# Performance work log

Hardware: AMD Instinct MI355X
Metric: run time of the kernel (lower is better)

The kernel has to match this reference:

```python
import jax, jax.numpy as jnp
import numpy as np

N_HEADS = 16
PROJ_DIM = 64  # per-head dim
DIM = N_HEADS * PROJ_DIM  # 1024


def setup_inputs() -> dict:
    key = jax.random.key(0)
    k1, k2, k3, k4, k5 = jax.random.split(key, 5)
    N, L = 2, 2048
    scale = 1.0 / np.sqrt(DIM)
    return {
        "query": jax.random.normal(k1, (N, L, DIM), dtype=jnp.float32),
        "key": jax.random.normal(k2, (N, L, DIM), dtype=jnp.float32),
        "Wq": jax.random.normal(k3, (DIM, DIM), dtype=jnp.float32) * scale,
        "Wk": jax.random.normal(k4, (DIM, DIM), dtype=jnp.float32) * scale,
        "Wv": jax.random.normal(k5, (DIM, DIM), dtype=jnp.float32) * scale,
    }


def reference(query, key, Wq, Wk, Wv):
    # Causal linear-complexity attention (mask=True branch, left_first=False).
    N, Lq, _ = query.shape
    Lk = key.shape[1]
    H, Dh = N_HEADS, PROJ_DIM
    # torch Linear: x @ W.T ; reshape to (N, H, L, Dh)
    q = (query @ Wq.T).reshape(N, Lq, H, Dh).transpose(0, 2, 1, 3)
    k = (key @ Wk.T).reshape(N, Lk, H, Dh).transpose(0, 2, 1, 3)
    v = (key @ Wv.T).reshape(N, Lk, H, Dh).transpose(0, 2, 1, 3)
    q = jax.nn.softmax(q, axis=-1)
    k = jax.nn.softmax(k, axis=-1)
    # right[t] = sum_{s<=t} k_s^T v_s  : (N,H,Lk,Dh,Dh) cumulative outer products
    S = jnp.cumsum(jnp.einsum('nhti,nhtj->nhtij', k, v), axis=2)
    out = jnp.einsum('nhti,nhtij->nhtj', q, S)  # (N,H,Lq,Dh)
    return out.transpose(0, 2, 1, 3).reshape(N, Lq, H * Dh)
```

## Files before the change

### kernel.cpp

```cpp
#include <hip/hip_runtime.h>


constexpr int DIM  = 1024;
constexpr int H    = 16;
constexpr int DH   = 64;
constexpr int LSEQ = 2048;
constexpr int NB   = 2;
constexpr int MTOK = NB * LSEQ;
constexpr int CS   = 64;
constexpr int NC   = LSEQ / CS;
constexpr int SEG  = 8;
constexpr int CPS  = NC / SEG;

typedef __bf16 bf16x8 __attribute__((ext_vector_type(8)));
typedef float floatx4 __attribute__((ext_vector_type(4)));
typedef unsigned short ushort_t;

__device__ __forceinline__ ushort_t f2bf(float f) {
  unsigned int u = __float_as_uint(f);
  u += 0x7FFFu + ((u >> 16) & 1u);
  return (ushort_t)(u >> 16);
}

__device__ __forceinline__ void async16(void* lds, const void* g) {
  __builtin_amdgcn_global_load_lds(
      (const __attribute__((address_space(1))) unsigned int*)g,
      (__attribute__((address_space(3))) unsigned int*)lds, 16, 0, 0);
}

__device__ __forceinline__ bf16x8 tfrag(const unsigned int* T, int row, int uoff) {
  union { bf16x8 v; unsigned int u[4]; } r;
  const unsigned int* p = T + row * 33 + uoff;
  r.u[0] = p[0]; r.u[1] = p[1]; r.u[2] = p[2]; r.u[3] = p[3];
  return r.v;
}

__device__ __forceinline__ void transpose_tile(const ushort_t* g, unsigned int* TT, int tid) {
  const int ic = tid & 7, tp = tid >> 3;
  const ushort_t* r0 = g + (size_t)(2 * tp) * DIM + ic * 8;
  union { uint4 q; ushort_t u[8]; } a0, a1;
  a0.q = *(const uint4*)r0;
  a1.q = *(const uint4*)(r0 + DIM);
#pragma unroll
  for (int j = 0; j < 8; j++)
    TT[(8 * ic + j) * 33 + tp] = (unsigned int)a0.u[j] | ((unsigned int)a1.u[j] << 16);
}

__global__ __launch_bounds__(256) void cast_all(const float* __restrict__ q,
                                                const float* __restrict__ k,
                                                const float* __restrict__ wq,
                                                const float* __restrict__ wk,
                                                const float* __restrict__ wv,
                                                ushort_t* __restrict__ xbf,
                                                ushort_t* __restrict__ wbf) {
  const int seg = blockIdx.y;
  const float* src;
  ushort_t* dst;
  int n4;
  if (seg == 0)      { src = q;  dst = xbf;                  n4 = (4 << 20) / 4; }
  else if (seg == 1) { src = k;  dst = xbf + (4 << 20);      n4 = (4 << 20) / 4; }
  else if (seg == 2) { src = wq; dst = wbf;                  n4 = (1 << 20) / 4; }
  else if (seg == 3) { src = wk; dst = wbf + (1 << 20);      n4 = (1 << 20) / 4; }
  else               { src = wv; dst = wbf + (2 << 20);      n4 = (1 << 20) / 4; }
  for (int i = blockIdx.x * 256 + threadIdx.x; i < n4; i += gridDim.x * 256) {
    const float4 f = ((const float4*)src)[i];
    ((ushort4*)dst)[i] = make_ushort4(f2bf(f.x), f2bf(f.y), f2bf(f.z), f2bf(f.w));
  }
}

__global__ __launch_bounds__(512, 2) void gemm_fused(const ushort_t* __restrict__ xbf,
                                                     const ushort_t* __restrict__ wbf,
                                                     ushort_t* __restrict__ qp,
                                                     ushort_t* __restrict__ kp,
                                                     ushort_t* __restrict__ vp) {
  __shared__ __align__(16) ushort_t sh[65536];
  const int tid = threadIdx.x;

  const int xcd   = blockIdx.x & 7;
  const int local = blockIdx.x >> 3;
  const int T     = xcd * 24 + local;
  const int z     = T >> 6;
  const int rem   = T & 63;
  const int bm    = (rem >> 2) * 256;
  const int bn    = (rem & 3) * 256;

  const ushort_t* A = xbf + (z ? (size_t)(4 << 20) : 0);
  const ushort_t* W = wbf + (size_t)z * (1 << 20);
  ushort_t* C = (z == 0) ? qp : ((z == 1) ? kp : vp);

  const int lane  = tid & 63;
  const int wid   = tid >> 6;
  const int wr    = wid >> 2, wc = wid & 3;
  const int row16 = lane & 15, quad = lane >> 4;

  floatx4 acc[8][4] = {};

  const int srow = tid >> 3;
  const int lc   = (tid & 7) ^ (srow & 7);
  const ushort_t* pA[2][2];
  const ushort_t* pB[2][2];
#pragma unroll
  for (int h = 0; h < 2; h++)
#pragma unroll
    for (int rnd = 0; rnd < 2; rnd++) {
      pA[h][rnd] = A + (size_t)(bm + h * 128 + rnd * 64 + srow) * DIM + lc * 8;
      pB[h][rnd] = W + (size_t)(bn + h * 128 + rnd * 64 + srow) * DIM + lc * 8;
    }
  char* shW = (char*)sh;

#define STG(b, ism, h, kt)                                          \
  {                                                                 \
    char* d_ = shW + (b) * 65536 + (ism) * 32768 + (h) * 16384 + tid * 16; \
    async16(d_,        ((ism) ? pB : pA)[h][0] + (size_t)(kt) * 64);       \
    async16(d_ + 8192, ((ism) ? pB : pA)[h][1] + (size_t)(kt) * 64);       \
  }

  const int key = row16 & 7;
  const int xc0 = (quad ^ key) * 16;
  const int xc1 = ((4 + quad) ^ key) * 16;
  const int aOff = wr * 16384 + row16 * 128;
  const int bOff = 32768 + (wc >> 1) * 16384 + (wc & 1) * 8192 + row16 * 128;
  const char* shR = (const char*)sh;

  bf16x8 aF[4][2], bF[4][2];

#define RD_A4(p, base)                                                        \
  {                                                                           \
    _Pragma("unroll")                                                         \
    for (int mt = 0; mt < 4; mt++) {                                          \
      aF[mt][0] = *(const bf16x8*)(shR + (p) * 65536 + aOff + ((base) + mt) * 2048 + xc0); \
      aF[mt][1] = *(const bf16x8*)(shR + (p) * 65536 + aOff + ((base) + mt) * 2048 + xc1); \
    }                                                                         \
  }
#define RD_B2(p, base)                                                        \
  {                                                                           \
    _Pragma("unroll")                                                         \
    for (int j = 0; j < 2; j++) {                                             \
      bF[(base) + j][0] = *(const bf16x8*)(shR + (p) * 65536 + bOff + ((base) + j) * 2048 + xc0); \
      bF[(base) + j][1] = *(const bf16x8*)(shR + (p) * 65536 + bOff + ((base) + j) * 2048 + xc1); \
    }                                                                         \
  }
#define MFMA8(mb, nb)                                                         \
  {                                                                           \
    _Pragma("unroll")                                                         \
    for (int mt = 0; mt < 4; mt++)                                            \
      _Pragma("unroll")                                                       \
      for (int nt = 0; nt < 2; nt++) {                                        \
        acc[(mb) + mt][(nb) + nt] = __builtin_amdgcn_mfma_f32_16x16x32_bf16(  \
            aF[mt][0], bF[(nb) + nt][0], acc[(mb) + mt][(nb) + nt], 0, 0, 0); \
        acc[(mb) + mt][(nb) + nt] = __builtin_amdgcn_mfma_f32_16x16x32_bf16(  \
            aF[mt][1], bF[(nb) + nt][1], acc[(mb) + mt][(nb) + nt], 0, 0, 0); \
      }                                                                       \
  }
#define BARD()  asm volatile("s_barrier" ::: "memory")
#define LGKM0() asm volatile("s_waitcnt lgkmcnt(0)" ::: "memory")

  STG(0, 0, 0, 0); STG(0, 1, 0, 0);
  STG(0, 1, 1, 0); STG(0, 0, 1, 0);
  STG(1, 0, 0, 1); STG(1, 1, 0, 1);
  asm volatile("s_waitcnt vmcnt(4)" ::: "memory");
  BARD();

  for (int u = 0; u < 16; ++u) {
    const int p  = u & 1;
    const int qb = p ^ 1;
    RD_A4(p, 0); RD_B2(p, 0);
    if (u + 1 < 16) { STG(qb, 1, 1, u + 1); STG(qb, 0, 1, u + 1); }
    BARD(); LGKM0();
    __builtin_amdgcn_s_setprio(1); MFMA8(0, 0); __builtin_amdgcn_s_setprio(0);
    BARD();
    RD_B2(p, 2);
    BARD(); LGKM0();
    __builtin_amdgcn_s_setprio(1); MFMA8(0, 2); __builtin_amdgcn_s_setprio(0);
    BARD();
    RD_A4(p, 4);
    BARD(); LGKM0();
    __builtin_amdgcn_s_setprio(1); MFMA8(4, 0); __builtin_amdgcn_s_setprio(0);
    BARD();
    if (u + 2 < 16) {
      STG(p, 0, 0, u + 2); STG(p, 1, 0, u + 2);
      asm volatile("s_waitcnt vmcnt(4)" ::: "memory");
    } else {
      asm volatile("s_waitcnt vmcnt(0)" ::: "memory");
    }
    BARD();
    __builtin_amdgcn_s_setprio(1); MFMA8(4, 2); __builtin_amdgcn_s_setprio(0);
    BARD();
  }
#undef STG
#undef RD_A4
#undef RD_B2
#undef MFMA8
#undef BARD
#undef LGKM0
  __syncthreads();

  if (z < 2) {
#pragma unroll
    for (int mt = 0; mt < 8; mt++)
#pragma unroll
      for (int r = 0; r < 4; r++) {
        float m = fmaxf(fmaxf(acc[mt][0][r], acc[mt][1][r]),
                        fmaxf(acc[mt][2][r], acc[mt][3][r]));
#pragma unroll
        for (int o = 1; o < 16; o <<= 1) m = fmaxf(m, __shfl_xor(m, o, 64));
        float e[4], s = 0.f;
#pragma unroll
        for (int nt = 0; nt < 4; nt++) { e[nt] = __expf(acc[mt][nt][r] - m); s += e[nt]; }
#pragma unroll
        for (int o = 1; o < 16; o <<= 1) s += __shfl_xor(s, o, 64);
        const float inv = 1.f / s;
#pragma unroll
        for (int nt = 0; nt < 4; nt++) acc[mt][nt][r] = e[nt] * inv;
      }
  }

  ushort_t* CsB = sh;
#pragma unroll
  for (int p4 = 0; p4 < 4; ++p4) {
    __syncthreads();
    if (wr == (p4 >> 1)) {
      const int mh = (p4 & 1) * 4;
#pragma unroll
      for (int m4 = 0; m4 < 4; m4++)
#pragma unroll
        for (int nt = 0; nt < 4; nt++)
#pragma unroll
          for (int r = 0; r < 4; r++)
            CsB[(m4 * 16 + quad * 4 + r) * 264 + wc * 64 + nt * 16 + row16] =
                f2bf(acc[mh + m4][nt][r]);
    }
    __syncthreads();
#pragma unroll
    for (int it = 0; it < 4; it++) {
      const int ch = tid + it * 512;
      const int row = ch >> 5, ic = ch & 31;
      *(uint4*)&C[(size_t)(bm + p4 * 64 + row) * DIM + bn + ic * 8] =
          *(const uint4*)&CsB[row * 264 + ic * 8];
    }
  }
}

__global__ __launch_bounds__(256) void seg_T(const ushort_t* __restrict__ kp,
                                             const ushort_t* __restrict__ vp,
                                             float* __restrict__ cs,
                                             float* __restrict__ segtot) {
  __shared__ unsigned int KT[64 * 33];
  __shared__ unsigned int VT[64 * 33];
  const int s = blockIdx.x, h = blockIdx.y, n = blockIdx.z;
  const int tid = threadIdx.x;
  const int lane = tid & 63, wid = tid >> 6;
  const int row16 = lane & 15, quad = lane >> 4;
  const int nh = n * H + h;

  floatx4 run[4] = {};
  for (int j = 0; j < CPS; j++) {
    const int c = s * CPS + j;
    const size_t gbase = ((size_t)(n * LSEQ + c * CS)) * DIM + h * DH;
    if (j) __syncthreads();
    transpose_tile(kp + gbase, KT, tid);
    transpose_tile(vp + gbase, VT, tid);
    __syncthreads();

    floatx4 tacc[4] = {};
#pragma unroll
    for (int ks = 0; ks < 2; ks++) {
      const bf16x8 a = tfrag(VT, wid * 16 + row16, ks * 16 + quad * 4);
#pragma unroll
      for (int nt = 0; nt < 4; nt++) {
        const bf16x8 b = tfrag(KT, nt * 16 + row16, ks * 16 + quad * 4);
        tacc[nt] = __builtin_amdgcn_mfma_f32_16x16x32_bf16(a, b, tacc[nt], 0, 0, 0);
      }
    }
    float* outp = cs + ((size_t)(nh * NC + c)) * (DH * DH);
#pragma unroll
    for (int nt = 0; nt < 4; nt++)
#pragma unroll
      for (int r = 0; r < 4; r++)
        outp[(wid * 16 + quad * 4 + r) * DH + nt * 16 + row16] = run[nt][r];
#pragma unroll
    for (int nt = 0; nt < 4; nt++) run[nt] += tacc[nt];
  }
  float* st = segtot + ((size_t)(nh * SEG + s)) * (DH * DH);
#pragma unroll
  for (int nt = 0; nt < 4; nt++)
#pragma unroll
    for (int r = 0; r < 4; r++)
      st[(wid * 16 + quad * 4 + r) * DH + nt * 16 + row16] = run[nt][r];
}

__global__ __launch_bounds__(512) void attn2(const ushort_t* __restrict__ qp,
                                             const ushort_t* __restrict__ kp,
                                             const ushort_t* __restrict__ vp,
                                             const float* __restrict__ cs,
                                             const float* __restrict__ segtot,
                                             float* __restrict__ out) {
  __shared__ float Sb[DH * DH];
  __shared__ ushort_t Qs[2][64 * 72];
  __shared__ ushort_t Ks[2][64 * 72];
  __shared__ ushort_t Ts[2][64 * 72];
  __shared__ ushort_t Pb[2][64 * 72];
  __shared__ unsigned int VT2[2][64 * 33];
  const int s = blockIdx.x, h = blockIdx.y, n = blockIdx.z;
  const int tid = threadIdx.x;
  const int half = tid >> 8;
  const int t8   = tid & 255;
  const int lane = tid & 63;
  const int wl   = (tid >> 6) & 3;
  const int row16 = lane & 15, quad = lane >> 4;
  const int nh = n * H + h;

  {
    float a8[8] = {0.f, 0.f, 0.f, 0.f, 0.f, 0.f, 0.f, 0.f};
    const float* base = segtot + (size_t)nh * SEG * (DH * DH) + tid * 8;
    for (int sp = 0; sp < s; sp++) {
      const float4 u0 = *(const float4*)(base + (size_t)sp * (DH * DH));
      const float4 u1 = *(const float4*)(base + (size_t)sp * (DH * DH) + 4);
      a8[0] += u0.x; a8[1] += u0.y; a8[2] += u0.z; a8[3] += u0.w;
      a8[4] += u1.x; a8[5] += u1.y; a8[6] += u1.z; a8[7] += u1.w;
    }
#pragma unroll
    for (int i = 0; i < 8; i++) Sb[tid * 8 + i] = a8[i];
  }
  __syncthreads();

  for (int r2 = 0; r2 < 2; r2++) {
    const int c = s * CPS + r2 * 2 + half;
    const size_t gbase = ((size_t)(n * LSEQ + c * CS)) * DIM + h * DH;
    const float* Pc = cs + ((size_t)(nh * NC + c)) * (DH * DH);
    if (r2) __syncthreads();

#pragma unroll
    for (int it = 0; it < 2; it++) {
      const int ch = t8 + it * 256;
      const int row = ch >> 3, ic = ch & 7;
      *(uint4*)&Qs[half][row * 72 + ic * 8] =
          *(const uint4*)&qp[gbase + (size_t)row * DIM + ic * 8];
      *(uint4*)&Ks[half][row * 72 + ic * 8] =
          *(const uint4*)&kp[gbase + (size_t)row * DIM + ic * 8];
    }
    transpose_tile(vp + gbase, VT2[half], t8);
#pragma unroll
    for (int ii = 0; ii < 2; ii++) {
      const int e = (t8 + ii * 256) * 8;
      const int row = e >> 6, col = e & 63;
      const float4 p0 = *(const float4*)(Pc + e);
      const float4 p1 = *(const float4*)(Pc + e + 4);
      ushort_t* d = &Ts[half][row * 72 + col];
      *(ushort4*)d = make_ushort4(f2bf(p0.x + Sb[e]),     f2bf(p0.y + Sb[e + 1]),
                                  f2bf(p0.z + Sb[e + 2]), f2bf(p0.w + Sb[e + 3]));
      *(ushort4*)(d + 4) = make_ushort4(f2bf(p1.x + Sb[e + 4]), f2bf(p1.y + Sb[e + 5]),
                                        f2bf(p1.z + Sb[e + 6]), f2bf(p1.w + Sb[e + 7]));
    }
    __syncthreads();

    const int t0 = wl * 16;
    floatx4 acc[4] = {};
    floatx4 pacc[4] = {};

#pragma unroll
    for (int ks = 0; ks < 2; ks++) {
      const bf16x8 aq = *(const bf16x8*)&Qs[half][(t0 + row16) * 72 + ks * 32 + quad * 8];
#pragma unroll
      for (int nt = 0; nt < 4; nt++) {
        const bf16x8 bt = *(const bf16x8*)&Ts[half][(nt * 16 + row16) * 72 + ks * 32 + quad * 8];
        acc[nt] = __builtin_amdgcn_mfma_f32_16x16x32_bf16(aq, bt, acc[nt], 0, 0, 0);
        const bf16x8 bk = *(const bf16x8*)&Ks[half][(nt * 16 + row16) * 72 + ks * 32 + quad * 8];
        pacc[nt] = __builtin_amdgcn_mfma_f32_16x16x32_bf16(aq, bk, pacc[nt], 0, 0, 0);
      }
    }
#pragma unroll
    for (int nt = 0; nt < 4; nt++)
#pragma unroll
      for (int r = 0; r < 4; r++) {
        const int tt = t0 + quad * 4 + r, ss = nt * 16 + row16;
        Pb[half][tt * 72 + ss] = f2bf((ss <= tt) ? pacc[nt][r] : 0.f);
      }
    __syncthreads();

#pragma unroll
    for (int ks = 0; ks < 2; ks++) {
      const bf16x8 ap = *(const bf16x8*)&Pb[half][(t0 + row16) * 72 + ks * 32 + quad * 8];
#pragma unroll
      for (int nt = 0; nt < 4; nt++) {
        const bf16x8 bv = tfrag(VT2[half], nt * 16 + row16, ks * 16 + quad * 4);
        acc[nt] = __builtin_amdgcn_mfma_f32_16x16x32_bf16(ap, bv, acc[nt], 0, 0, 0);
      }
    }

#pragma unroll
    for (int nt = 0; nt < 4; nt++)
#pragma unroll
      for (int r = 0; r < 4; r++)
        out[gbase + (size_t)(t0 + quad * 4 + r) * DIM + nt * 16 + row16] = acc[nt][r];
  }
}

extern "C" void kernel_launch(void* const* d_in, const int* in_sizes, int n_in,
                              void* d_out, int out_size, void* d_ws, size_t ws_size,
                              hipStream_t stream) {
  const float* query = (const float*)d_in[0];
  const float* key   = (const float*)d_in[1];
  const float* Wq    = (const float*)d_in[2];
  const float* Wk    = (const float*)d_in[3];
  const float* Wv    = (const float*)d_in[4];
  float* out = (float*)d_out;

  const size_t PM = (size_t)4 << 20;
  ushort_t* qp = (ushort_t*)d_ws;
  ushort_t* kp = qp + PM;
  ushort_t* vp = kp + PM;
  float*    cs = (float*)(vp + PM);
  float*    segtot = cs + PM;
  ushort_t* xbf = (ushort_t*)cs;
  ushort_t* wbf = (ushort_t*)out;

  cast_all<<<dim3(512, 5), 256, 0, stream>>>(query, key, Wq, Wk, Wv, xbf, wbf);

  gemm_fused<<<dim3(192), 512, 0, stream>>>(xbf, wbf, qp, kp, vp);

  seg_T<<<dim3(SEG, H, NB), 256, 0, stream>>>(kp, vp, cs, segtot);

  attn2<<<dim3(SEG, H, NB), 512, 0, stream>>>(qp, kp, vp, cs, segtot, out);
}
```

Measured before the change: 156.2 us.

## Process all four chunks per segment in parallel with 1024-thread blocks

```diff
diff --git a/kernel.cpp b/kernel.cpp
--- a/kernel.cpp
+++ b/kernel.cpp
@@ -241,159 +241,172 @@
   }
 }
 
-__global__ __launch_bounds__(256) void seg_T(const ushort_t* __restrict__ kp,
-                                             const ushort_t* __restrict__ vp,
-                                             float* __restrict__ cs,
-                                             float* __restrict__ segtot) {
-  __shared__ unsigned int KT[64 * 33];
-  __shared__ unsigned int VT[64 * 33];
+__global__ __launch_bounds__(1024, 1) void seg_T(const ushort_t* __restrict__ kp,
+                                                 const ushort_t* __restrict__ vp,
+                                                 float* __restrict__ cs,
+                                                 float* __restrict__ segtot) {
+  __shared__ unsigned int KT[4][64 * 33];
+  __shared__ unsigned int VT[4][64 * 33];
+  __shared__ float Tsl[3][DH * DH];
   const int s = blockIdx.x, h = blockIdx.y, n = blockIdx.z;
   const int tid = threadIdx.x;
-  const int lane = tid & 63, wid = tid >> 6;
+  const int qd  = tid >> 8;
+  const int t8  = tid & 255;
+  const int lane = tid & 63;
+  const int wid  = (tid >> 6) & 3;
   const int row16 = lane & 15, quad = lane >> 4;
   const int nh = n * H + h;
-
-  floatx4 run[4] = {};
-  for (int j = 0; j < CPS; j++) {
-    const int c = s * CPS + j;
-    const size_t gbase = ((size_t)(n * LSEQ + c * CS)) * DIM + h * DH;
-    if (j) __syncthreads();
-    transpose_tile(kp + gbase, KT, tid);
-    transpose_tile(vp + gbase, VT, tid);
-    __syncthreads();
-
-    floatx4 tacc[4] = {};
-#pragma unroll
-    for (int ks = 0; ks < 2; ks++) {
-      const bf16x8 a = tfrag(VT, wid * 16 + row16, ks * 16 + quad * 4);
-#pragma unroll
-      for (int nt = 0; nt < 4; nt++) {
-        const bf16x8 b = tfrag(KT, nt * 16 + row16, ks * 16 + quad * 4);
-        tacc[nt] = __builtin_amdgcn_mfma_f32_16x16x32_bf16(a, b, tacc[nt], 0, 0, 0);
+  const int c  = s * CPS + qd;
+  const size_t gbase = ((size_t)(n * LSEQ + c * CS)) * DIM + h * DH;
+
+  transpose_tile(kp + gbase, KT[qd], t8);
+  transpose_tile(vp + gbase, VT[qd], t8);
+  __syncthreads();
+
+  floatx4 tacc[4] = {};
+#pragma unroll
+  for (int ks = 0; ks < 2; ks++) {
+    const bf16x8 a = tfrag(VT[qd], wid * 16 + row16, ks * 16 + quad * 4);
+#pragma unroll
+    for (int nt = 0; nt < 4; nt++) {
+      const bf16x8 b = tfrag(KT[qd], nt * 16 + row16, ks * 16 + quad * 4);
+      tacc[nt] = __builtin_amdgcn_mfma_f32_16x16x32_bf16(a, b, tacc[nt], 0, 0, 0);
+    }
+  }
+  if (qd < 3) {
+#pragma unroll
+    for (int nt = 0; nt < 4; nt++)
+#pragma unroll
+      for (int r = 0; r < 4; r++)
+        Tsl[qd][(wid * 16 + quad * 4 + r) * DH + nt * 16 + row16] = tacc[nt][r];
+  }
+  __syncthreads();
+
+  float* outp = cs + ((size_t)(nh * NC + c)) * (DH * DH);
+#pragma unroll
+  for (int nt = 0; nt < 4; nt++)
+#pragma unroll
+    for (int r = 0; r < 4; r++) {
+      const int pos = (wid * 16 + quad * 4 + r) * DH + nt * 16 + row16;
+      float p = 0.f;
+      if (qd > 0) p += Tsl[0][pos];
+      if (qd > 1) p += Tsl[1][pos];
+      if (qd > 2) p += Tsl[2][pos];
+      outp[pos] = p;
+      if (qd == 3) {
+        segtot[((size_t)(nh * SEG + s)) * (DH * DH) + pos] = p + tacc[nt][r];
       }
     }
-    float* outp = cs + ((size_t)(nh * NC + c)) * (DH * DH);
-#pragma unroll
-    for (int nt = 0; nt < 4; nt++)
-#pragma unroll
-      for (int r = 0; r < 4; r++)
-        outp[(wid * 16 + quad * 4 + r) * DH + nt * 16 + row16] = run[nt][r];
-#pragma unroll
-    for (int nt = 0; nt < 4; nt++) run[nt] += tacc[nt];
-  }
-  float* st = segtot + ((size_t)(nh * SEG + s)) * (DH * DH);
-#pragma unroll
-  for (int nt = 0; nt < 4; nt++)
-#pragma unroll
-    for (int r = 0; r < 4; r++)
-      st[(wid * 16 + quad * 4 + r) * DH + nt * 16 + row16] = run[nt][r];
-}
-
-__global__ __launch_bounds__(512) void attn2(const ushort_t* __restrict__ qp,
-                                             const ushort_t* __restrict__ kp,
-                                             const ushort_t* __restrict__ vp,
-                                             const float* __restrict__ cs,
-                                             const float* __restrict__ segtot,
-                                             float* __restrict__ out) {
-  __shared__ float Sb[DH * DH];
-  __shared__ ushort_t Qs[2][64 * 72];
-  __shared__ ushort_t Ks[2][64 * 72];
-  __shared__ ushort_t Ts[2][64 * 72];
-  __shared__ ushort_t Pb[2][64 * 72];
-  __shared__ unsigned int VT2[2][64 * 33];
+}
+
+__global__ __launch_bounds__(1024, 1) void attn2(const ushort_t* __restrict__ qp,
+                                                 const ushort_t* __restrict__ kp,
+                                                 const ushort_t* __restrict__ vp,
+                                                 const float* __restrict__ cs,
+                                                 const float* __restrict__ segtot,
+                                                 float* __restrict__ out) {
+  __shared__ ushort_t Qs[4][64 * 72];
+  __shared__ ushort_t Ks[4][64 * 72];
+  __shared__ ushort_t TsPb[4][64 * 72];
+  __shared__ unsigned int VT2[4][64 * 33];
   const int s = blockIdx.x, h = blockIdx.y, n = blockIdx.z;
   const int tid = threadIdx.x;
-  const int half = tid >> 8;
-  const int t8   = tid & 255;
+  const int qd  = tid >> 8;
+  const int t8  = tid & 255;
   const int lane = tid & 63;
   const int wl   = (tid >> 6) & 3;
   const int row16 = lane & 15, quad = lane >> 4;
   const int nh = n * H + h;
-
+  const int c  = s * CPS + qd;
+  const size_t gbase = ((size_t)(n * LSEQ + c * CS)) * DIM + h * DH;
+  const float* Pc = cs + ((size_t)(nh * NC + c)) * (DH * DH);
+
+  float sb[16] = {0.f, 0.f, 0.f, 0.f, 0.f, 0.f, 0.f, 0.f,
+                  0.f, 0.f, 0.f, 0.f, 0.f, 0.f, 0.f, 0.f};
   {
-    float a8[8] = {0.f, 0.f, 0.f, 0.f, 0.f, 0.f, 0.f, 0.f};
-    const float* base = segtot + (size_t)nh * SEG * (DH * DH) + tid * 8;
+    const float* base = segtot + (size_t)nh * SEG * (DH * DH);
     for (int sp = 0; sp < s; sp++) {
-      const float4 u0 = *(const float4*)(base + (size_t)sp * (DH * DH));
-      const float4 u1 = *(const float4*)(base + (size_t)sp * (DH * DH) + 4);
-      a8[0] += u0.x; a8[1] += u0.y; a8[2] += u0.z; a8[3] += u0.w;
-      a8[4] += u1.x; a8[5] += u1.y; a8[6] += u1.z; a8[7] += u1.w;
-    }
-#pragma unroll
-    for (int i = 0; i < 8; i++) Sb[tid * 8 + i] = a8[i];
-  }
-  __syncthreads();
-
-  for (int r2 = 0; r2 < 2; r2++) {
-    const int c = s * CPS + r2 * 2 + half;
-    const size_t gbase = ((size_t)(n * LSEQ + c * CS)) * DIM + h * DH;
-    const float* Pc = cs + ((size_t)(nh * NC + c)) * (DH * DH);
-    if (r2) __syncthreads();
-
-#pragma unroll
-    for (int it = 0; it < 2; it++) {
-      const int ch = t8 + it * 256;
-      const int row = ch >> 3, ic = ch & 7;
-      *(uint4*)&Qs[half][row * 72 + ic * 8] =
-          *(const uint4*)&qp[gbase + (size_t)row * DIM + ic * 8];
-      *(uint4*)&Ks[half][row * 72 + ic * 8] =
-          *(const uint4*)&kp[gbase + (size_t)row * DIM + ic * 8];
-    }
-    transpose_tile(vp + gbase, VT2[half], t8);
-#pragma unroll
-    for (int ii = 0; ii < 2; ii++) {
-      const int e = (t8 + ii * 256) * 8;
-      const int row = e >> 6, col = e & 63;
-      const float4 p0 = *(const float4*)(Pc + e);
-      const float4 p1 = *(const float4*)(Pc + e + 4);
-      ushort_t* d = &Ts[half][row * 72 + col];
-      *(ushort4*)d = make_ushort4(f2bf(p0.x + Sb[e]),     f2bf(p0.y + Sb[e + 1]),
-                                  f2bf(p0.z + Sb[e + 2]), f2bf(p0.w + Sb[e + 3]));
-      *(ushort4*)(d + 4) = make_ushort4(f2bf(p1.x + Sb[e + 4]), f2bf(p1.y + Sb[e + 5]),
-                                        f2bf(p1.z + Sb[e + 6]), f2bf(p1.w + Sb[e + 7]));
-    }
-    __syncthreads();
-
-    const int t0 = wl * 16;
-    floatx4 acc[4] = {};
-    floatx4 pacc[4] = {};
-
-#pragma unroll
-    for (int ks = 0; ks < 2; ks++) {
-      const bf16x8 aq = *(const bf16x8*)&Qs[half][(t0 + row16) * 72 + ks * 32 + quad * 8];
-#pragma unroll
-      for (int nt = 0; nt < 4; nt++) {
-        const bf16x8 bt = *(const bf16x8*)&Ts[half][(nt * 16 + row16) * 72 + ks * 32 + quad * 8];
-        acc[nt] = __builtin_amdgcn_mfma_f32_16x16x32_bf16(aq, bt, acc[nt], 0, 0, 0);
-        const bf16x8 bk = *(const bf16x8*)&Ks[half][(nt * 16 + row16) * 72 + ks * 32 + quad * 8];
-        pacc[nt] = __builtin_amdgcn_mfma_f32_16x16x32_bf16(aq, bk, pacc[nt], 0, 0, 0);
+      const float* bsp = base + (size_t)sp * (DH * DH);
+#pragma unroll
+      for (int ii = 0; ii < 2; ii++) {
+        const int e = (t8 + ii * 256) * 8;
+        const float4 u0 = *(const float4*)(bsp + e);
+        const float4 u1 = *(const float4*)(bsp + e + 4);
+        sb[ii * 8 + 0] += u0.x; sb[ii * 8 + 1] += u0.y;
+        sb[ii * 8 + 2] += u0.z; sb[ii * 8 + 3] += u0.w;
+        sb[ii * 8 + 4] += u1.x; sb[ii * 8 + 5] += u1.y;
+        sb[ii * 8 + 6] += u1.z; sb[ii * 8 + 7] += u1.w;
       }
     }
-#pragma unroll
-    for (int nt = 0; nt < 4; nt++)
-#pragma unroll
-      for (int r = 0; r < 4; r++) {
-        const int tt = t0 + quad * 4 + r, ss = nt * 16 + row16;
-        Pb[half][tt * 72 + ss] = f2bf((ss <= tt) ? pacc[nt][r] : 0.f);
-      }
-    __syncthreads();
-
-#pragma unroll
-    for (int ks = 0; ks < 2; ks++) {
-      const bf16x8 ap = *(const bf16x8*)&Pb[half][(t0 + row16) * 72 + ks * 32 + quad * 8];
-#pragma unroll
-      for (int nt = 0; nt < 4; nt++) {
-        const bf16x8 bv = tfrag(VT2[half], nt * 16 + row16, ks * 16 + quad * 4);
-        acc[nt] = __builtin_amdgcn_mfma_f32_16x16x32_bf16(ap, bv, acc[nt], 0, 0, 0);
-      }
-    }
-
-#pragma unroll
-    for (int nt = 0; nt < 4; nt++)
-#pragma unroll
-      for (int r = 0; r < 4; r++)
-        out[gbase + (size_t)(t0 + quad * 4 + r) * DIM + nt * 16 + row16] = acc[nt][r];
-  }
+  }
+
+#pragma unroll
+  for (int it = 0; it < 2; it++) {
+    const int ch = t8 + it * 256;
+    const int row = ch >> 3, ic = ch & 7;
+    *(uint4*)&Qs[qd][row * 72 + ic * 8] =
+        *(const uint4*)&qp[gbase + (size_t)row * DIM + ic * 8];
+    *(uint4*)&Ks[qd][row * 72 + ic * 8] =
+        *(const uint4*)&kp[gbase + (size_t)row * DIM + ic * 8];
+  }
+  transpose_tile(vp + gbase, VT2[qd], t8);
+#pragma unroll
+  for (int ii = 0; ii < 2; ii++) {
+    const int e = (t8 + ii * 256) * 8;
+    const int row = e >> 6, col = e & 63;
+    const float4 p0 = *(const float4*)(Pc + e);
+    const float4 p1 = *(const float4*)(Pc + e + 4);
+    ushort_t* d = &TsPb[qd][row * 72 + col];
+    *(ushort4*)d = make_ushort4(
+        f2bf(p0.x + sb[ii * 8 + 0]), f2bf(p0.y + sb[ii * 8 + 1]),
+        f2bf(p0.z + sb[ii * 8 + 2]), f2bf(p0.w + sb[ii * 8 + 3]));
+    *(ushort4*)(d + 4) = make_ushort4(
+        f2bf(p1.x + sb[ii * 8 + 4]), f2bf(p1.y + sb[ii * 8 + 5]),
+        f2bf(p1.z + sb[ii * 8 + 6]), f2bf(p1.w + sb[ii * 8 + 7]));
+  }
+  __syncthreads();
+
+  const int t0 = wl * 16;
+  floatx4 acc[4] = {};
+  floatx4 pacc[4] = {};
+
+#pragma unroll
+  for (int ks = 0; ks < 2; ks++) {
+    const bf16x8 aq = *(const bf16x8*)&Qs[qd][(t0 + row16) * 72 + ks * 32 + quad * 8];
+#pragma unroll
+    for (int nt = 0; nt < 4; nt++) {
+      const bf16x8 bt = *(const bf16x8*)&TsPb[qd][(nt * 16 + row16) * 72 + ks * 32 + quad * 8];
+      acc[nt] = __builtin_amdgcn_mfma_f32_16x16x32_bf16(aq, bt, acc[nt], 0, 0, 0);
+      const bf16x8 bk = *(const bf16x8*)&Ks[qd][(nt * 16 + row16) * 72 + ks * 32 + quad * 8];
+      pacc[nt] = __builtin_amdgcn_mfma_f32_16x16x32_bf16(aq, bk, pacc[nt], 0, 0, 0);
+    }
+  }
+  __syncthreads();
+
+#pragma unroll
+  for (int nt = 0; nt < 4; nt++)
+#pragma unroll
+    for (int r = 0; r < 4; r++) {
+      const int tt = t0 + quad * 4 + r, ss = nt * 16 + row16;
+      TsPb[qd][tt * 72 + ss] = f2bf((ss <= tt) ? pacc[nt][r] : 0.f);
+    }
+  __syncthreads();
+
+#pragma unroll
+  for (int ks = 0; ks < 2; ks++) {
+    const bf16x8 ap = *(const bf16x8*)&TsPb[qd][(t0 + row16) * 72 + ks * 32 + quad * 8];
+#pragma unroll
+    for (int nt = 0; nt < 4; nt++) {
+      const bf16x8 bv = tfrag(VT2[qd], nt * 16 + row16, ks * 16 + quad * 4);
+      acc[nt] = __builtin_amdgcn_mfma_f32_16x16x32_bf16(ap, bv, acc[nt], 0, 0, 0);
+    }
+  }
+
+#pragma unroll
+  for (int nt = 0; nt < 4; nt++)
+#pragma unroll
+    for (int r = 0; r < 4; r++)
+      out[gbase + (size_t)(t0 + quad * 4 + r) * DIM + nt * 16 + row16] = acc[nt][r];
 }
 
 extern "C" void kernel_launch(void* const* d_in, const int* in_sizes, int n_in,
@@ -419,7 +432,7 @@
 
   gemm_fused<<<dim3(192), 512, 0, stream>>>(xbf, wbf, qp, kp, vp);
 
-  seg_T<<<dim3(SEG, H, NB), 256, 0, stream>>>(kp, vp, cs, segtot);
-
-  attn2<<<dim3(SEG, H, NB), 512, 0, stream>>>(qp, kp, vp, cs, segtot, out);
-}
+  seg_T<<<dim3(SEG, H, NB), 1024, 0, stream>>>(kp, vp, cs, segtot);
+
+  attn2<<<dim3(SEG, H, NB), 1024, 0, stream>>>(qp, kp, vp, cs, segtot, out);
+}
```

After: 160.3 us (median of 2 runs). +2.6%, slower.
